# Kernel optimization log

Hardware: AMD Instinct MI355X
Metric: run time of the kernel (lower is better)

The kernel has to match this reference:

```python
import jax, jax.numpy as jnp
import numpy as np
import math

FILT_LEN = 10  # all Farras / dual filters are 10-tap
INV_SQRT2 = 1.0 / math.sqrt(2.0)

# Farras first-stage analysis filters (fs_farras), shape [tree(2), lo/hi(2), 10]
_F = 0.08838834764832
_G = 0.01122679215254
_H = 0.69587998903400
FAF_NP = np.array([
    [[0.0, -_F, _F, _H, _H, _F, -_F, _G, _G, 0.0],
     [0.0, -_G, _G, _F, _F, -_H, _H, -_F, -_F, 0.0]],
    [[_G, _G, -_F, _F, _H, _H, _F, -_F, 0.0, 0.0],
     [0.0, 0.0, -_F, -_F, _H, -_H, _F, _F, _G, -_G]]], dtype=np.float32)
# Kingsbury Q-shift dual filters (duelfilt / dualfilt1), shape [tree(2), lo/hi(2), 10]
_A = 0.03516384
_B = 0.08832942
_C = 0.23389032
_D = 0.76027237
_E = 0.58751830
_K = 0.11430184
AF_NP = np.array([
    [[_A, 0.0, -_B, _C, _D, _E, 0.0, -_K, 0.0, 0.0],
     [0.0, 0.0, -_K, 0.0, _E, -_D, _C, _B, 0.0, -_A]],
    [[0.0, 0.0, -_K, 0.0, _E, _D, _C, -_B, 0.0, _A],
     [-_A, 0.0, _B, _C, -_D, _E, 0.0, -_K, 0.0, 0.0]]], dtype=np.float32)


def _afb_axis(x, lo_f, hi_f, axis):
    """1D circular analysis filter bank along spatial `axis` (1=rows, 2=cols).
    x: (B,H,W,C). Returns (lo, hi), each halved along `axis`.
    Math: x <- cshift(x,-L); y = downsample2(fullconv(x,f)); wrap-add first L taps.
    """
    N = x.shape[axis]
    L = FILT_LEN // 2
    C = x.shape[-1]
    x = jnp.roll(x, -L, axis=axis)

    def conv(f):
        kf = f[::-1].astype(x.dtype)  # lax does correlation -> flip for convolution
        if axis == 1:
            ker = jnp.tile(kf.reshape(FILT_LEN, 1, 1, 1), (1, 1, 1, C))
            pad = [(FILT_LEN - 1, FILT_LEN - 1), (0, 0)]
            strides = (2, 1)
        else:
            ker = jnp.tile(kf.reshape(1, FILT_LEN, 1, 1), (1, 1, 1, C))
            pad = [(0, 0), (FILT_LEN - 1, FILT_LEN - 1)]
            strides = (1, 2)
        return jax.lax.conv_general_dilated(
            x, ker, window_strides=strides, padding=pad,
            dimension_numbers=('NHWC', 'HWIO', 'NHWC'),
            feature_group_count=C)  # depthwise, per-channel identical filter

    def wrap(y):
        # y has N//2 + L samples along axis; fold periodic tail into head
        head = (jax.lax.slice_in_dim(y, 0, L, axis=axis)
                + jax.lax.slice_in_dim(y, N // 2, N // 2 + L, axis=axis))
        body = jax.lax.slice_in_dim(y, L, N // 2, axis=axis)
        return jnp.concatenate([head, body], axis=axis)

    return wrap(conv(lo_f)), wrap(conv(hi_f))


def afb2d(x, lo_row, hi_row, lo_col, hi_col):
    """2D separable analysis filter bank: returns (lo, [lohi, hilo, hihi])."""
    Lr, Hr = _afb_axis(x, lo_row, hi_row, axis=1)
    lo, w0 = _afb_axis(Lr, lo_col, hi_col, axis=2)
    w1, w2 = _afb_axis(Hr, lo_col, hi_col, axis=2)
    return lo, [w0, w1, w2]


def _add_sub(a, b):
    return (a + b) * INV_SQRT2, (a - b) * INV_SQRT2


def _dtcwt(x, Faf, af, level):
    x = x / 2
    w = [[[None, None] for _ in range(2)] for _ in range(level + 1)]
    for m in range(2):
        for n in range(2):
            lo, w[0][m][n] = afb2d(x, Faf[m, 0], Faf[m, 1], Faf[n, 0], Faf[n, 1])
            for j in range(1, level):
                lo, w[j][m][n] = afb2d(lo, af[m, 0], af[m, 1], af[n, 0], af[n, 1])
            w[level][m][n] = lo
    # combine dual trees into (approx) complex pairs
    for j in range(level):
        for s in range(3):
            w[j][0][0][s], w[j][1][1][s] = _add_sub(w[j][0][0][s], w[j][1][1][s])
            w[j][0][1][s], w[j][1][0][s] = _add_sub(w[j][0][1][s], w[j][1][0][s])
    # multiscale 2x2 tiling reassembly (concat=True path)
    wc = w
    for j in range(level - 1, 0, -1):
        for a in range(2):
            for b in range(2):
                wc[j][a][b] = jnp.concatenate([
                    jnp.concatenate([wc[j + 1][a][b], wc[j][a][b][0]], axis=2),
                    jnp.concatenate([wc[j][a][b][1], wc[j][a][b][2]], axis=2)], axis=1)
    tiles = []
    for a in range(2):
        for b in range(2):
            tiles.append(jnp.concatenate([
                jnp.concatenate([wc[1][a][b], wc[0][a][b][0]], axis=2),
                jnp.concatenate([wc[0][a][b][1], wc[0][a][b][2]], axis=2)], axis=1))
    w0, w1, w2, w3 = tiles
    return jnp.concatenate([jnp.concatenate([w0, w1], axis=2),
                            jnp.concatenate([w2, w3], axis=2)], axis=1)


def setup_inputs() -> dict:
    key = jax.random.key(0)
    x = jax.random.normal(key, (8, 512, 512, 3), dtype=jnp.float32)
    return {"x": x, "Faf": jnp.asarray(FAF_NP), "af": jnp.asarray(AF_NP), "level": 3}


def reference(x, Faf, af, level):
    return _dtcwt(x, Faf, af, int(level))
```

## Files before the change

kernel.cpp:

```cpp
#include <hip/hip_runtime.h>


#define FF 0.08838834764832f
#define GG 0.01122679215254f
#define HHc 0.69587998903400f
#define AAc 0.03516384f
#define BBc 0.08832942f
#define CCc 0.23389032f
#define DDc 0.76027237f
#define EEc 0.58751830f
#define KKc 0.11430184f

__device__ __constant__ float c_filt[2][2][2][10] = {
  {
    { {0.f,-FF, FF, HHc, HHc, FF,-FF, GG, GG, 0.f},
      {0.f,-GG, GG, FF, FF,-HHc, HHc,-FF,-FF, 0.f} },
    { {GG, GG,-FF, FF, HHc, HHc, FF,-FF, 0.f, 0.f},
      {0.f, 0.f,-FF,-FF, HHc,-HHc, FF, FF, GG,-GG} }
  },
  {
    { {AAc, 0.f,-BBc, CCc, DDc, EEc, 0.f,-KKc, 0.f, 0.f},
      {0.f, 0.f,-KKc, 0.f, EEc,-DDc, CCc, BBc, 0.f,-AAc} },
    { {0.f, 0.f,-KKc, 0.f, EEc, DDc, CCc,-BBc, 0.f, AAc},
      {-AAc, 0.f, BBc, CCc,-DDc, EEc, 0.f,-KKc, 0.f, 0.f} }
  }
};

__device__ __forceinline__ void cmb(float& a, float& b) {
  const float k = 0.70710678118654752440f;
  const float s = (a + b) * k, d = (a - b) * k;
  a = s; b = d;
}

__device__ __forceinline__ int swz4(int f4) { return f4 ^ ((f4 >> 3) & 7); }

template<int N, int Ho, int Wo, int NT>
__global__ __launch_bounds__(NT) void fused_level0(
    const float* __restrict__ src,
    float* __restrict__ llout,
    float* __restrict__ out)
{
  constexpr int half = N / 2;
  constexpr int W2 = 2 * Wo + 8;
  constexpr int ROWF = 3 * N;
  constexpr int FL = 3 * W2;
  constexpr int I4 = FL / 4;
  constexpr int RR = 2 * Ho + 8;
  constexpr int SIF4 = 3 * W2 + 4;
  constexpr size_t ZOUT = (size_t)8 * half * half * 3;
  static_assert(Ho * Wo * 2 == NT, "stage-B thread map (z-pair split)");
  __shared__ __align__(16) float raw[RR * FL];
  __shared__ __align__(16) float inter[Ho * SIF4 * 4];

  const int jt = blockIdx.x, it = blockIdx.y, b = blockIdx.z;
  const int i0 = it * Ho, j0 = jt * Wo;
  const int tid = threadIdx.x;

  int base = (2 * j0 - 4) * 3;
  if (base < 0) base += ROWF;

  const float* sb = src + (size_t)b * N * ROWF;
  for (int item = tid; item < RR * I4; item += NT) {
    const int lr = item / I4;
    const int q4 = (item - lr * I4) * 4;
    int fg = base + q4;
    if (fg >= ROWF) fg -= ROWF;
    const int g = (2 * i0 - 4 + lr) & (N - 1);
    *(float4*)&raw[lr * FL + q4] = *(const float4*)(sb + (size_t)g * ROWF + fg);
  }
  __syncthreads();

  for (int item = tid; item < Ho * I4; item += NT) {
    const int il = item / I4;
    const int q4 = (item - il * I4) * 4;
    float acc[4][4];
#pragma unroll
    for (int f = 0; f < 4; ++f)
#pragma unroll
      for (int k = 0; k < 4; ++k) acc[f][k] = 0.f;
#pragma unroll
    for (int t = 0; t < 10; ++t) {
      const int lr = 2 * il + 9 - t;
      const float4 v = *(const float4*)&raw[lr * FL + q4];
#pragma unroll
      for (int f = 0; f < 4; ++f) {
        const float fc = c_filt[0][f >> 1][f & 1][t];
        acc[f][0] += fc * v.x; acc[f][1] += fc * v.y;
        acc[f][2] += fc * v.z; acc[f][3] += fc * v.w;
      }
    }
#pragma unroll
    for (int f = 0; f < 4; ++f)
#pragma unroll
      for (int k = 0; k < 4; ++k) acc[f][k] *= 0.5f;
#pragma unroll
    for (int k = 0; k < 4; ++k) {
      const int fq = q4 + k;
      float4 w = make_float4(acc[0][k], acc[1][k], acc[2][k], acc[3][k]);
      *(float4*)&inter[(il * SIF4 + swz4(fq)) * 4] = w;
    }
  }
  __syncthreads();

  {
    const int pr = (tid >= Ho * Wo) ? 1 : 0;
    const int t7 = tid - pr * Ho * Wo;
    const int il = t7 / Wo, jl = t7 - (t7 / Wo) * Wo;
    const int za = pr, zb = 3 - pr;
    float LLa[3] = {}, LHa[3] = {}, HLa[3] = {}, HHa[3] = {};
    float LLb[3] = {}, LHb[3] = {}, HLb[3] = {}, HHb[3] = {};
#pragma unroll
    for (int s = 0; s < 10; ++s) {
      const int wl = 2 * jl + 9 - s;
      const float fla = c_filt[0][pr][0][s],     fha = c_filt[0][pr][1][s];
      const float flb = c_filt[0][1 - pr][0][s], fhb = c_filt[0][1 - pr][1][s];
#pragma unroll
      for (int c = 0; c < 3; ++c) {
        const int f4 = wl * 3 + c;
        const float4 v = *(const float4*)&inter[(il * SIF4 + swz4(f4)) * 4];
        const float aa = v.x, da = v.y, ab = v.z, db = v.w;
        LLa[c] += fla * aa; LHa[c] += fha * aa;
        HLa[c] += fla * da; HHa[c] += fha * da;
        LLb[c] += flb * ab; LHb[c] += fhb * ab;
        HLb[c] += flb * db; HHb[c] += fhb * db;
      }
    }
#pragma unroll
    for (int c = 0; c < 3; ++c) {
      cmb(LHa[c], LHb[c]); cmb(HLa[c], HLb[c]); cmb(HHa[c], HHb[c]);
    }
    const int ig = i0 + il, jg = j0 + jl;
    const size_t outB = (size_t)b * (1024u * 1024u * 3u);
    {
      const int m = za >> 1, n = za & 1;
      const int r0 = m * 512, c0 = n * 512;
      float* pLL = llout + (size_t)za * ZOUT + (((size_t)b * half + ig) * half + jg) * 3;
      pLL[0] = LLa[0]; pLL[1] = LLa[1]; pLL[2] = LLa[2];
      float* pLH = out + outB + ((size_t)(r0 + ig) * 1024 + (c0 + half + jg)) * 3;
      pLH[0] = LHa[0]; pLH[1] = LHa[1]; pLH[2] = LHa[2];
      float* pHL = out + outB + ((size_t)(r0 + half + ig) * 1024 + (c0 + jg)) * 3;
      pHL[0] = HLa[0]; pHL[1] = HLa[1]; pHL[2] = HLa[2];
      float* pHH = out + outB + ((size_t)(r0 + half + ig) * 1024 + (c0 + half + jg)) * 3;
      pHH[0] = HHa[0]; pHH[1] = HHa[1]; pHH[2] = HHa[2];
    }
    {
      const int m = zb >> 1, n = zb & 1;
      const int r0 = m * 512, c0 = n * 512;
      float* pLL = llout + (size_t)zb * ZOUT + (((size_t)b * half + ig) * half + jg) * 3;
      pLL[0] = LLb[0]; pLL[1] = LLb[1]; pLL[2] = LLb[2];
      float* pLH = out + outB + ((size_t)(r0 + ig) * 1024 + (c0 + half + jg)) * 3;
      pLH[0] = LHb[0]; pLH[1] = LHb[1]; pLH[2] = LHb[2];
      float* pHL = out + outB + ((size_t)(r0 + half + ig) * 1024 + (c0 + jg)) * 3;
      pHL[0] = HLb[0]; pHL[1] = HLb[1]; pHL[2] = HLb[2];
      float* pHH = out + outB + ((size_t)(r0 + half + ig) * 1024 + (c0 + half + jg)) * 3;
      pHH[0] = HHb[0]; pHH[1] = HHb[1]; pHH[2] = HHb[2];
    }
  }
}

template<int LVL, int N, int Ho, int Wo, int NT>
__global__ __launch_bounds__(NT) void fused_level(
    const float* __restrict__ src,
    float* __restrict__ llout,
    float* __restrict__ out)
{
  constexpr int half = N / 2;
  constexpr int W2 = 2 * Wo + 8;
  constexpr int NF = 8;
  constexpr int ROWF = 3 * N;
  constexpr int FL = 3 * W2;
  constexpr int SIF4 = (3 * W2 * NF) / 4 + 4;
  constexpr size_t ZS = (size_t)8 * N * N * 3;
  constexpr size_t ZOUT = (size_t)8 * half * half * 3;
  static_assert(Ho * Wo * 2 == NT, "stage-B thread map (z-pair split)");
  __shared__ __align__(16) float inter[Ho * SIF4 * 4];

  const int jt = blockIdx.x, it = blockIdx.y, b = blockIdx.z;
  const int i0 = it * Ho, j0 = jt * Wo;
  const int tid = threadIdx.x;

  int base = (2 * j0 - 4) * 3;
  if (base < 0) base += ROWF;

  constexpr int I4 = FL / 4;
  for (int item = tid; item < Ho * I4; item += NT) {
    const int il = item / I4;
    const int q4 = (item - il * I4) * 4;
    int fg = base + q4;
    if (fg >= ROWF) fg -= ROWF;
    const int ig = i0 + il;
    float acc[NF][4];
#pragma unroll
    for (int f = 0; f < NF; ++f)
#pragma unroll
      for (int k = 0; k < 4; ++k) acc[f][k] = 0.f;

#pragma unroll
    for (int z = 0; z < 4; ++z) {
      const int m = z >> 1;
      const float* sp = src + (size_t)z * ZS + (size_t)b * N * ROWF + fg;
#pragma unroll
      for (int t = 0; t < 10; ++t) {
        const int r = (2 * ig + 5 - t) & (N - 1);
        const float4 v = *(const float4*)(sp + (size_t)r * ROWF);
        const float fl = c_filt[1][m][0][t], fh = c_filt[1][m][1][t];
        acc[2 * z][0] += fl * v.x; acc[2 * z][1] += fl * v.y;
        acc[2 * z][2] += fl * v.z; acc[2 * z][3] += fl * v.w;
        acc[2 * z + 1][0] += fh * v.x; acc[2 * z + 1][1] += fh * v.y;
        acc[2 * z + 1][2] += fh * v.z; acc[2 * z + 1][3] += fh * v.w;
      }
    }
#pragma unroll
    for (int k = 0; k < 4; ++k) {
      const int fq = q4 + k;
      float4 w0 = make_float4(acc[0][k], acc[1][k], acc[2][k], acc[3][k]);
      float4 w1 = make_float4(acc[4][k], acc[5][k], acc[6][k], acc[7][k]);
      *(float4*)&inter[(il * SIF4 + swz4(2 * fq)) * 4] = w0;
      *(float4*)&inter[(il * SIF4 + swz4(2 * fq + 1)) * 4] = w1;
    }
  }
  __syncthreads();

  {
    const int pr = (tid >= Ho * Wo) ? 1 : 0;
    const int t7 = tid - pr * Ho * Wo;
    const int il = t7 / Wo, jl = t7 - (t7 / Wo) * Wo;
    const int za = pr, zb = 3 - pr;
    float LLa[3] = {}, LHa[3] = {}, HLa[3] = {}, HHa[3] = {};
    float LLb[3] = {}, LHb[3] = {}, HLb[3] = {}, HHb[3] = {};
#pragma unroll
    for (int s = 0; s < 10; ++s) {
      const int wl = 2 * jl + 9 - s;
      const float fla = c_filt[1][pr][0][s],     fha = c_filt[1][pr][1][s];
      const float flb = c_filt[1][1 - pr][0][s], fhb = c_filt[1][1 - pr][1][s];
#pragma unroll
      for (int c = 0; c < 3; ++c) {
        const int f4 = (wl * 3 + c) * 2;
        const float4 v0 = *(const float4*)&inter[(il * SIF4 + swz4(f4)) * 4];
        const float4 v1 = *(const float4*)&inter[(il * SIF4 + swz4(f4 + 1)) * 4];
        const float aa = pr ? v0.z : v0.x, da = pr ? v0.w : v0.y;
        const float ab = pr ? v1.x : v1.z, db = pr ? v1.y : v1.w;
        LLa[c] += fla * aa; LHa[c] += fha * aa;
        HLa[c] += fla * da; HHa[c] += fha * da;
        LLb[c] += flb * ab; LHb[c] += fhb * ab;
        HLb[c] += flb * db; HHb[c] += fhb * db;
      }
    }
#pragma unroll
    for (int c = 0; c < 3; ++c) {
      cmb(LHa[c], LHb[c]); cmb(HLa[c], HLb[c]); cmb(HHa[c], HHb[c]);
    }
    const int ig = i0 + il, jg = j0 + jl;
    const size_t outB = (size_t)b * (1024u * 1024u * 3u);
    {
      const int m = za >> 1, n = za & 1;
      const int r0 = m * 512, c0 = n * 512;
      float* pLL;
      if constexpr (LVL == 2)
        pLL = out + outB + ((size_t)(r0 + ig) * 1024 + (c0 + jg)) * 3;
      else
        pLL = llout + (size_t)za * ZOUT + (((size_t)b * half + ig) * half + jg) * 3;
      pLL[0] = LLa[0]; pLL[1] = LLa[1]; pLL[2] = LLa[2];
      float* pLH = out + outB + ((size_t)(r0 + ig) * 1024 + (c0 + half + jg)) * 3;
      pLH[0] = LHa[0]; pLH[1] = LHa[1]; pLH[2] = LHa[2];
      float* pHL = out + outB + ((size_t)(r0 + half + ig) * 1024 + (c0 + jg)) * 3;
      pHL[0] = HLa[0]; pHL[1] = HLa[1]; pHL[2] = HLa[2];
      float* pHH = out + outB + ((size_t)(r0 + half + ig) * 1024 + (c0 + half + jg)) * 3;
      pHH[0] = HHa[0]; pHH[1] = HHa[1]; pHH[2] = HHa[2];
    }
    {
      const int m = zb >> 1, n = zb & 1;
      const int r0 = m * 512, c0 = n * 512;
      float* pLL;
      if constexpr (LVL == 2)
        pLL = out + outB + ((size_t)(r0 + ig) * 1024 + (c0 + jg)) * 3;
      else
        pLL = llout + (size_t)zb * ZOUT + (((size_t)b * half + ig) * half + jg) * 3;
      pLL[0] = LLb[0]; pLL[1] = LLb[1]; pLL[2] = LLb[2];
      float* pLH = out + outB + ((size_t)(r0 + ig) * 1024 + (c0 + half + jg)) * 3;
      pLH[0] = LHb[0]; pLH[1] = LHb[1]; pLH[2] = LHb[2];
      float* pHL = out + outB + ((size_t)(r0 + half + ig) * 1024 + (c0 + jg)) * 3;
      pHL[0] = HLb[0]; pHL[1] = HLb[1]; pHL[2] = HLb[2];
      float* pHH = out + outB + ((size_t)(r0 + half + ig) * 1024 + (c0 + half + jg)) * 3;
      pHH[0] = HHb[0]; pHH[1] = HHb[1]; pHH[2] = HHb[2];
    }
  }
}

extern "C" void kernel_launch(void* const* d_in, const int* in_sizes, int n_in,
                              void* d_out, int out_size, void* d_ws, size_t ws_size,
                              hipStream_t stream) {
  (void)in_sizes; (void)n_in; (void)out_size; (void)ws_size;
  const float* x = (const float*)d_in[0];
  float* out = (float*)d_out;
  float* LL1 = (float*)d_ws;
  float* LL2 = LL1 + 6291456;

  fused_level0<512, 4, 32, 256><<<dim3(8, 64, 8), 256, 0, stream>>>(x, LL1, out);
  fused_level<1, 256, 8, 16, 256><<<dim3(8, 16, 8), 256, 0, stream>>>(LL1, LL2, out);
  fused_level<2, 128, 8, 16, 256><<<dim3(4, 8, 8), 256, 0, stream>>>(LL2, nullptr, out);
}
```

Measured before the change: 184.9 us.

## Double-buffer level-0 tiles with async global-to-LDS loads; remap stage-B threads

The level-0 kernel now handles two vertically adjacent row tiles per block. It issues the second tile's global loads straight into a second LDS buffer via global_load_lds, so they overlap the first tile's row and column filtering. Levels 1 and 2 change their column stage so each of half the threads computes all four trees, instead of all threads computing a tree pair. The trade-offs are double the raw LDS per block, half the level-0 grid, and fewer active threads in the level-1/2 column stage. The async loads also rely on barriers being enough to order the DMA writes to LDS before they are read.

```diff
diff --git a/kernel.cpp b/kernel.cpp
--- a/kernel.cpp
+++ b/kernel.cpp
@@ -34,42 +34,47 @@
 
 __device__ __forceinline__ int swz4(int f4) { return f4 ^ ((f4 >> 3) & 7); }
 
+#if defined(__has_builtin)
+#if __has_builtin(__builtin_amdgcn_global_load_lds)
+#define G2L_ASYNC 1
+#endif
+#endif
+
+__device__ __forceinline__ void g2l16(const float* g, float* l) {
+#ifdef G2L_ASYNC
+  typedef const __attribute__((address_space(1))) float gfl;
+  typedef __attribute__((address_space(3))) float lfl;
+  __builtin_amdgcn_global_load_lds((gfl*)g, (lfl*)l, 16, 0, 0);
+#else
+  *(float4*)l = *(const float4*)g;
+#endif
+}
+
 template<int N, int Ho, int Wo, int NT>
-__global__ __launch_bounds__(NT) void fused_level0(
-    const float* __restrict__ src,
-    float* __restrict__ llout,
-    float* __restrict__ out)
-{
-  constexpr int half = N / 2;
-  constexpr int W2 = 2 * Wo + 8;
+__device__ __forceinline__ void l0_issue(const float* sb, int i0, int base,
+                                         float* rawbuf, int tid) {
   constexpr int ROWF = 3 * N;
+  constexpr int W2 = 2 * Wo + 8;
   constexpr int FL = 3 * W2;
   constexpr int I4 = FL / 4;
   constexpr int RR = 2 * Ho + 8;
-  constexpr int SIF4 = 3 * W2 + 4;
-  constexpr size_t ZOUT = (size_t)8 * half * half * 3;
-  static_assert(Ho * Wo * 2 == NT, "stage-B thread map (z-pair split)");
-  __shared__ __align__(16) float raw[RR * FL];
-  __shared__ __align__(16) float inter[Ho * SIF4 * 4];
-
-  const int jt = blockIdx.x, it = blockIdx.y, b = blockIdx.z;
-  const int i0 = it * Ho, j0 = jt * Wo;
-  const int tid = threadIdx.x;
-
-  int base = (2 * j0 - 4) * 3;
-  if (base < 0) base += ROWF;
-
-  const float* sb = src + (size_t)b * N * ROWF;
   for (int item = tid; item < RR * I4; item += NT) {
     const int lr = item / I4;
     const int q4 = (item - lr * I4) * 4;
     int fg = base + q4;
     if (fg >= ROWF) fg -= ROWF;
     const int g = (2 * i0 - 4 + lr) & (N - 1);
-    *(float4*)&raw[lr * FL + q4] = *(const float4*)(sb + (size_t)g * ROWF + fg);
-  }
-  __syncthreads();
-
+    g2l16(sb + (size_t)g * ROWF + fg, rawbuf + (size_t)item * 4);
+  }
+}
+
+template<int N, int Ho, int Wo, int NT>
+__device__ __forceinline__ void l0_rowfilt(const float* raw, float* inter,
+                                           int tid) {
+  constexpr int W2 = 2 * Wo + 8;
+  constexpr int FL = 3 * W2;
+  constexpr int I4 = FL / 4;
+  constexpr int SIF4 = 3 * W2 + 4;
   for (int item = tid; item < Ho * I4; item += NT) {
     const int il = item / I4;
     const int q4 = (item - il * I4) * 4;
@@ -100,79 +105,125 @@
       *(float4*)&inter[(il * SIF4 + swz4(fq)) * 4] = w;
     }
   }
-  __syncthreads();
-
+}
+
+template<int N, int Ho, int Wo, int NT>
+__device__ __forceinline__ void l0_colfilt(const float* inter, int i0, int j0,
+                                           int b, int tid,
+                                           float* __restrict__ llout,
+                                           float* __restrict__ out) {
+  constexpr int half = N / 2;
+  constexpr int W2 = 2 * Wo + 8;
+  constexpr int SIF4 = 3 * W2 + 4;
+  constexpr size_t ZOUT = (size_t)8 * half * half * 3;
+  const int pr = (tid >= Ho * Wo) ? 1 : 0;
+  const int t7 = tid - pr * Ho * Wo;
+  const int il = t7 / Wo, jl = t7 - (t7 / Wo) * Wo;
+  const int za = pr, zb = 3 - pr;
+  float LLa[3] = {}, LHa[3] = {}, HLa[3] = {}, HHa[3] = {};
+  float LLb[3] = {}, LHb[3] = {}, HLb[3] = {}, HHb[3] = {};
+#pragma unroll
+  for (int s = 0; s < 10; ++s) {
+    const int wl = 2 * jl + 9 - s;
+    const float fla = c_filt[0][pr][0][s],     fha = c_filt[0][pr][1][s];
+    const float flb = c_filt[0][1 - pr][0][s], fhb = c_filt[0][1 - pr][1][s];
+#pragma unroll
+    for (int c = 0; c < 3; ++c) {
+      const int f4 = wl * 3 + c;
+      const float4 v = *(const float4*)&inter[(il * SIF4 + swz4(f4)) * 4];
+      const float aa = v.x, da = v.y, ab = v.z, db = v.w;
+      LLa[c] += fla * aa; LHa[c] += fha * aa;
+      HLa[c] += fla * da; HHa[c] += fha * da;
+      LLb[c] += flb * ab; LHb[c] += fhb * ab;
+      HLb[c] += flb * db; HHb[c] += fhb * db;
+    }
+  }
+#pragma unroll
+  for (int c = 0; c < 3; ++c) {
+    cmb(LHa[c], LHb[c]); cmb(HLa[c], HLb[c]); cmb(HHa[c], HHb[c]);
+  }
+  const int ig = i0 + il, jg = j0 + jl;
+  const size_t outB = (size_t)b * (1024u * 1024u * 3u);
   {
-    const int pr = (tid >= Ho * Wo) ? 1 : 0;
-    const int t7 = tid - pr * Ho * Wo;
-    const int il = t7 / Wo, jl = t7 - (t7 / Wo) * Wo;
-    const int za = pr, zb = 3 - pr;
-    float LLa[3] = {}, LHa[3] = {}, HLa[3] = {}, HHa[3] = {};
-    float LLb[3] = {}, LHb[3] = {}, HLb[3] = {}, HHb[3] = {};
-#pragma unroll
-    for (int s = 0; s < 10; ++s) {
-      const int wl = 2 * jl + 9 - s;
-      const float fla = c_filt[0][pr][0][s],     fha = c_filt[0][pr][1][s];
-      const float flb = c_filt[0][1 - pr][0][s], fhb = c_filt[0][1 - pr][1][s];
-#pragma unroll
-      for (int c = 0; c < 3; ++c) {
-        const int f4 = wl * 3 + c;
-        const float4 v = *(const float4*)&inter[(il * SIF4 + swz4(f4)) * 4];
-        const float aa = v.x, da = v.y, ab = v.z, db = v.w;
-        LLa[c] += fla * aa; LHa[c] += fha * aa;
-        HLa[c] += fla * da; HHa[c] += fha * da;
-        LLb[c] += flb * ab; LHb[c] += fhb * ab;
-        HLb[c] += flb * db; HHb[c] += fhb * db;
-      }
-    }
-#pragma unroll
-    for (int c = 0; c < 3; ++c) {
-      cmb(LHa[c], LHb[c]); cmb(HLa[c], HLb[c]); cmb(HHa[c], HHb[c]);
-    }
-    const int ig = i0 + il, jg = j0 + jl;
-    const size_t outB = (size_t)b * (1024u * 1024u * 3u);
-    {
-      const int m = za >> 1, n = za & 1;
-      const int r0 = m * 512, c0 = n * 512;
-      float* pLL = llout + (size_t)za * ZOUT + (((size_t)b * half + ig) * half + jg) * 3;
-      pLL[0] = LLa[0]; pLL[1] = LLa[1]; pLL[2] = LLa[2];
-      float* pLH = out + outB + ((size_t)(r0 + ig) * 1024 + (c0 + half + jg)) * 3;
-      pLH[0] = LHa[0]; pLH[1] = LHa[1]; pLH[2] = LHa[2];
-      float* pHL = out + outB + ((size_t)(r0 + half + ig) * 1024 + (c0 + jg)) * 3;
-      pHL[0] = HLa[0]; pHL[1] = HLa[1]; pHL[2] = HLa[2];
-      float* pHH = out + outB + ((size_t)(r0 + half + ig) * 1024 + (c0 + half + jg)) * 3;
-      pHH[0] = HHa[0]; pHH[1] = HHa[1]; pHH[2] = HHa[2];
-    }
-    {
-      const int m = zb >> 1, n = zb & 1;
-      const int r0 = m * 512, c0 = n * 512;
-      float* pLL = llout + (size_t)zb * ZOUT + (((size_t)b * half + ig) * half + jg) * 3;
-      pLL[0] = LLb[0]; pLL[1] = LLb[1]; pLL[2] = LLb[2];
-      float* pLH = out + outB + ((size_t)(r0 + ig) * 1024 + (c0 + half + jg)) * 3;
-      pLH[0] = LHb[0]; pLH[1] = LHb[1]; pLH[2] = LHb[2];
-      float* pHL = out + outB + ((size_t)(r0 + half + ig) * 1024 + (c0 + jg)) * 3;
-      pHL[0] = HLb[0]; pHL[1] = HLb[1]; pHL[2] = HLb[2];
-      float* pHH = out + outB + ((size_t)(r0 + half + ig) * 1024 + (c0 + half + jg)) * 3;
-      pHH[0] = HHb[0]; pHH[1] = HHb[1]; pHH[2] = HHb[2];
-    }
-  }
-}
-
-template<int LVL, int N, int Ho, int Wo, int NT>
-__global__ __launch_bounds__(NT) void fused_level(
+    const int m = za >> 1, n = za & 1;
+    const int r0 = m * 512, c0 = n * 512;
+    float* pLL = llout + (size_t)za * ZOUT + (((size_t)b * half + ig) * half + jg) * 3;
+    pLL[0] = LLa[0]; pLL[1] = LLa[1]; pLL[2] = LLa[2];
+    float* pLH = out + outB + ((size_t)(r0 + ig) * 1024 + (c0 + half + jg)) * 3;
+    pLH[0] = LHa[0]; pLH[1] = LHa[1]; pLH[2] = LHa[2];
+    float* pHL = out + outB + ((size_t)(r0 + half + ig) * 1024 + (c0 + jg)) * 3;
+    pHL[0] = HLa[0]; pHL[1] = HLa[1]; pHL[2] = HLa[2];
+    float* pHH = out + outB + ((size_t)(r0 + half + ig) * 1024 + (c0 + half + jg)) * 3;
+    pHH[0] = HHa[0]; pHH[1] = HHa[1]; pHH[2] = HHa[2];
+  }
+  {
+    const int m = zb >> 1, n = zb & 1;
+    const int r0 = m * 512, c0 = n * 512;
+    float* pLL = llout + (size_t)zb * ZOUT + (((size_t)b * half + ig) * half + jg) * 3;
+    pLL[0] = LLb[0]; pLL[1] = LLb[1]; pLL[2] = LLb[2];
+    float* pLH = out + outB + ((size_t)(r0 + ig) * 1024 + (c0 + half + jg)) * 3;
+    pLH[0] = LHb[0]; pLH[1] = LHb[1]; pLH[2] = LHb[2];
+    float* pHL = out + outB + ((size_t)(r0 + half + ig) * 1024 + (c0 + jg)) * 3;
+    pHL[0] = HLb[0]; pHL[1] = HLb[1]; pHL[2] = HLb[2];
+    float* pHH = out + outB + ((size_t)(r0 + half + ig) * 1024 + (c0 + half + jg)) * 3;
+    pHH[0] = HHb[0]; pHH[1] = HHb[1]; pHH[2] = HHb[2];
+  }
+}
+
+template<int N, int Ho, int Wo, int NT>
+__global__ __launch_bounds__(NT) void fused_level0_pipe(
+    const float* __restrict__ src,
+    float* __restrict__ llout,
+    float* __restrict__ out)
+{
+  constexpr int W2 = 2 * Wo + 8;
+  constexpr int ROWF = 3 * N;
+  constexpr int FL = 3 * W2;
+  constexpr int RR = 2 * Ho + 8;
+  constexpr int SIF4 = 3 * W2 + 4;
+  static_assert(Ho * Wo * 2 == NT, "stage-B thread map (z-pair split)");
+  __shared__ __align__(16) float raw0[RR * FL];
+  __shared__ __align__(16) float raw1[RR * FL];
+  __shared__ __align__(16) float inter[Ho * SIF4 * 4];
+
+  const int jt = blockIdx.x, ity = blockIdx.y, b = blockIdx.z;
+  const int j0 = jt * Wo;
+  const int i0a = (2 * ity) * Ho;
+  const int i0b = i0a + Ho;
+  const int tid = threadIdx.x;
+  int base = (2 * j0 - 4) * 3;
+  if (base < 0) base += ROWF;
+  const float* sb = src + (size_t)b * N * ROWF;
+
+  l0_issue<N, Ho, Wo, NT>(sb, i0a, base, raw0, tid);
+  __syncthreads();
+  l0_issue<N, Ho, Wo, NT>(sb, i0b, base, raw1, tid);
+#ifdef G2L_ASYNC
+  __builtin_amdgcn_sched_barrier(0);
+#endif
+  l0_rowfilt<N, Ho, Wo, NT>(raw0, inter, tid);
+  __syncthreads();
+  l0_colfilt<N, Ho, Wo, NT>(inter, i0a, j0, b, tid, llout, out);
+  __syncthreads();
+  l0_rowfilt<N, Ho, Wo, NT>(raw1, inter, tid);
+  __syncthreads();
+  l0_colfilt<N, Ho, Wo, NT>(inter, i0b, j0, b, tid, llout, out);
+}
+
+template<int LVL, int N, int Ho, int Wo>
+__global__ __launch_bounds__(256) void fused_level(
     const float* __restrict__ src,
     float* __restrict__ llout,
     float* __restrict__ out)
 {
   constexpr int half = N / 2;
   constexpr int W2 = 2 * Wo + 8;
-  constexpr int NF = 8;
+  constexpr int NF = (LVL == 0) ? 4 : 8;
   constexpr int ROWF = 3 * N;
   constexpr int FL = 3 * W2;
   constexpr int SIF4 = (3 * W2 * NF) / 4 + 4;
   constexpr size_t ZS = (size_t)8 * N * N * 3;
   constexpr size_t ZOUT = (size_t)8 * half * half * 3;
-  static_assert(Ho * Wo * 2 == NT, "stage-B thread map (z-pair split)");
   __shared__ __align__(16) float inter[Ho * SIF4 * 4];
 
   const int jt = blockIdx.x, it = blockIdx.y, b = blockIdx.z;
@@ -183,7 +234,7 @@
   if (base < 0) base += ROWF;
 
   constexpr int I4 = FL / 4;
-  for (int item = tid; item < Ho * I4; item += NT) {
+  for (int item = tid; item < Ho * I4; item += 256) {
     const int il = item / I4;
     const int q4 = (item - il * I4) * 4;
     int fg = base + q4;
@@ -221,68 +272,52 @@
   }
   __syncthreads();
 
-  {
-    const int pr = (tid >= Ho * Wo) ? 1 : 0;
-    const int t7 = tid - pr * Ho * Wo;
-    const int il = t7 / Wo, jl = t7 - (t7 / Wo) * Wo;
-    const int za = pr, zb = 3 - pr;
-    float LLa[3] = {}, LHa[3] = {}, HLa[3] = {}, HHa[3] = {};
-    float LLb[3] = {}, LHb[3] = {}, HLb[3] = {}, HHb[3] = {};
+  if (tid < Ho * Wo) {
+    const int il = tid / Wo, jl = tid - (tid / Wo) * Wo;
+    float LL[4][3] = {}, LH[4][3] = {}, HL[4][3] = {}, HH[4][3] = {};
 #pragma unroll
     for (int s = 0; s < 10; ++s) {
       const int wl = 2 * jl + 9 - s;
-      const float fla = c_filt[1][pr][0][s],     fha = c_filt[1][pr][1][s];
-      const float flb = c_filt[1][1 - pr][0][s], fhb = c_filt[1][1 - pr][1][s];
 #pragma unroll
       for (int c = 0; c < 3; ++c) {
         const int f4 = (wl * 3 + c) * 2;
         const float4 v0 = *(const float4*)&inter[(il * SIF4 + swz4(f4)) * 4];
         const float4 v1 = *(const float4*)&inter[(il * SIF4 + swz4(f4 + 1)) * 4];
-        const float aa = pr ? v0.z : v0.x, da = pr ? v0.w : v0.y;
-        const float ab = pr ? v1.x : v1.z, db = pr ? v1.y : v1.w;
-        LLa[c] += fla * aa; LHa[c] += fha * aa;
-        HLa[c] += fla * da; HHa[c] += fha * da;
-        LLb[c] += flb * ab; LHb[c] += fhb * ab;
-        HLb[c] += flb * db; HHb[c] += fhb * db;
+        const float az[4] = {v0.x, v0.z, v1.x, v1.z};
+        const float dz[4] = {v0.y, v0.w, v1.y, v1.w};
+#pragma unroll
+        for (int z = 0; z < 4; ++z) {
+          const int n = z & 1;
+          const float fl = c_filt[1][n][0][s], fh = c_filt[1][n][1][s];
+          LL[z][c] += fl * az[z]; LH[z][c] += fh * az[z];
+          HL[z][c] += fl * dz[z]; HH[z][c] += fh * dz[z];
+        }
       }
     }
 #pragma unroll
     for (int c = 0; c < 3; ++c) {
-      cmb(LHa[c], LHb[c]); cmb(HLa[c], HLb[c]); cmb(HHa[c], HHb[c]);
+      cmb(LH[0][c], LH[3][c]); cmb(LH[1][c], LH[2][c]);
+      cmb(HL[0][c], HL[3][c]); cmb(HL[1][c], HL[2][c]);
+      cmb(HH[0][c], HH[3][c]); cmb(HH[1][c], HH[2][c]);
     }
     const int ig = i0 + il, jg = j0 + jl;
     const size_t outB = (size_t)b * (1024u * 1024u * 3u);
-    {
-      const int m = za >> 1, n = za & 1;
+#pragma unroll
+    for (int z = 0; z < 4; ++z) {
+      const int m = z >> 1, n = z & 1;
       const int r0 = m * 512, c0 = n * 512;
       float* pLL;
       if constexpr (LVL == 2)
         pLL = out + outB + ((size_t)(r0 + ig) * 1024 + (c0 + jg)) * 3;
       else
-        pLL = llout + (size_t)za * ZOUT + (((size_t)b * half + ig) * half + jg) * 3;
-      pLL[0] = LLa[0]; pLL[1] = LLa[1]; pLL[2] = LLa[2];
+        pLL = llout + (size_t)z * ZOUT + (((size_t)b * half + ig) * half + jg) * 3;
+      pLL[0] = LL[z][0]; pLL[1] = LL[z][1]; pLL[2] = LL[z][2];
       float* pLH = out + outB + ((size_t)(r0 + ig) * 1024 + (c0 + half + jg)) * 3;
-      pLH[0] = LHa[0]; pLH[1] = LHa[1]; pLH[2] = LHa[2];
+      pLH[0] = LH[z][0]; pLH[1] = LH[z][1]; pLH[2] = LH[z][2];
       float* pHL = out + outB + ((size_t)(r0 + half + ig) * 1024 + (c0 + jg)) * 3;
-      pHL[0] = HLa[0]; pHL[1] = HLa[1]; pHL[2] = HLa[2];
+      pHL[0] = HL[z][0]; pHL[1] = HL[z][1]; pHL[2] = HL[z][2];
       float* pHH = out + outB + ((size_t)(r0 + half + ig) * 1024 + (c0 + half + jg)) * 3;
-      pHH[0] = HHa[0]; pHH[1] = HHa[1]; pHH[2] = HHa[2];
-    }
-    {
-      const int m = zb >> 1, n = zb & 1;
-      const int r0 = m * 512, c0 = n * 512;
-      float* pLL;
-      if constexpr (LVL == 2)
-        pLL = out + outB + ((size_t)(r0 + ig) * 1024 + (c0 + jg)) * 3;
-      else
-        pLL = llout + (size_t)zb * ZOUT + (((size_t)b * half + ig) * half + jg) * 3;
-      pLL[0] = LLb[0]; pLL[1] = LLb[1]; pLL[2] = LLb[2];
-      float* pLH = out + outB + ((size_t)(r0 + ig) * 1024 + (c0 + half + jg)) * 3;
-      pLH[0] = LHb[0]; pLH[1] = LHb[1]; pLH[2] = LHb[2];
-      float* pHL = out + outB + ((size_t)(r0 + half + ig) * 1024 + (c0 + jg)) * 3;
-      pHL[0] = HLb[0]; pHL[1] = HLb[1]; pHL[2] = HLb[2];
-      float* pHH = out + outB + ((size_t)(r0 + half + ig) * 1024 + (c0 + half + jg)) * 3;
-      pHH[0] = HHb[0]; pHH[1] = HHb[1]; pHH[2] = HHb[2];
+      pHH[0] = HH[z][0]; pHH[1] = HH[z][1]; pHH[2] = HH[z][2];
     }
   }
 }
@@ -296,7 +331,7 @@
   float* LL1 = (float*)d_ws;
   float* LL2 = LL1 + 6291456;
 
-  fused_level0<512, 4, 32, 256><<<dim3(8, 64, 8), 256, 0, stream>>>(x, LL1, out);
-  fused_level<1, 256, 8, 16, 256><<<dim3(8, 16, 8), 256, 0, stream>>>(LL1, LL2, out);
-  fused_level<2, 128, 8, 16, 256><<<dim3(4, 8, 8), 256, 0, stream>>>(LL2, nullptr, out);
-}
+  fused_level0_pipe<512, 4, 32, 256><<<dim3(8, 32, 8), 256, 0, stream>>>(x, LL1, out);
+  fused_level<1, 256, 8, 16><<<dim3(8, 16, 8), 256, 0, stream>>>(LL1, LL2, out);
+  fused_level<2, 128, 8, 16><<<dim3(4, 8, 8), 256, 0, stream>>>(LL2, nullptr, out);
+}
```

Result: faster. 171.1 us (-7.5%).
